# Performance work log

Hardware: AMD Instinct MI355X
Metric: run time of the kernel (lower is better)

## Reference

```python
import jax, jax.numpy as jnp
import numpy as np

B, FIN, FOUT, FH = 32, 32, 32, 64
H = W = 128
LAT = 512
K_IN, K_MID, K_OUT, K_SHORT = FH * FIN, FH * FH, FOUT * FH, FOUT * FIN
K_TOTAL = K_IN + K_MID + K_OUT + K_SHORT + FH + FH + FOUT + FOUT  # 9408


def setup_inputs() -> dict:
    key = jax.random.key(0)
    ks = jax.random.split(key, 20)
    def rn(k, shape, scale=None):
        s = scale if scale is not None else 1.0 / np.sqrt(shape[-1])
        return jax.random.normal(k, shape, dtype=jnp.float32) * s
    return {
        "x": jax.random.normal(ks[0], (B, FIN, H, W), dtype=jnp.float32),
        "lat": jax.random.normal(ks[1], (B, LAT), dtype=jnp.float32),
        "w0": rn(ks[2], (LAT, LAT)), "b0": rn(ks[3], (LAT,), 0.02),
        "w1a": rn(ks[4], (2 * LAT, LAT)), "b1a": rn(ks[5], (2 * LAT,), 0.02),
        "w1b": rn(ks[6], (LAT, 2 * LAT)), "b1b": rn(ks[7], (LAT,), 0.02),
        "w1s": rn(ks[8], (LAT, LAT)), "b1s": rn(ks[9], (LAT,), 0.02),
        "w2a": rn(ks[10], (2 * LAT, LAT)), "b2a": rn(ks[11], (2 * LAT,), 0.02),
        "w2b": rn(ks[12], (K_TOTAL, 2 * LAT)), "b2b": rn(ks[13], (K_TOTAL,), 0.02),
        "w2s": rn(ks[14], (K_TOTAL, LAT)), "b2s": rn(ks[15], (K_TOTAL,), 0.02),
        "wfa": rn(ks[16], (K_TOTAL, K_TOTAL)), "bfa": rn(ks[17], (K_TOTAL,), 0.02),
    }


def _lrb(h, wa, ba, wb, bb, ws, bs):
    # LinearResidualBlock: shortcut + 2-layer MLP with ReLU
    return h @ ws.T + bs + jax.nn.relu(h @ wa.T + ba) @ wb.T + bb


def reference(x, lat, w0, b0, w1a, b1a, w1b, b1b, w1s, b1s,
              w2a, b2a, w2b, b2b, w2s, b2s, wfa, bfa):
    # hypernetwork: dyna_k then LinearFA (forward is a plain linear)
    h = lat @ w0.T + b0                              # [B, 512]
    h = _lrb(h, w1a, b1a, w1b, b1b, w1s, b1s)        # [B, 512]
    h = _lrb(h, w2a, b2a, w2b, b2b, w2s, b2s)        # [B, K_TOTAL]
    ks = h @ wfa.T + bfa                             # [B, K_TOTAL]

    sizes = [K_IN, K_MID, K_OUT, K_SHORT, FH, FH, FOUT, FOUT]
    offs = np.cumsum([0] + sizes)
    k_in = ks[:, offs[0]:offs[1]].reshape(B, FH, FIN)
    k_mid = ks[:, offs[1]:offs[2]].reshape(B, FH, FH)
    k_out = ks[:, offs[2]:offs[3]].reshape(B, FOUT, FH)
    k_short = ks[:, offs[3]:offs[4]].reshape(B, FOUT, FIN)
    b_in = ks[:, offs[4]:offs[5]][:, :, None, None]    # [B, FH, 1, 1]
    b_mid = ks[:, offs[5]:offs[6]][:, :, None, None]
    b_out = ks[:, offs[6]:offs[7]][:, :, None, None]   # [B, FOUT, 1, 1]
    b_short = ks[:, offs[7]:offs[8]][:, :, None, None]

    # per-sample 1x1 grouped convs == batched matmuls over channels
    xs = jnp.einsum('bihw,boi->bohw', x, k_short) + b_short
    xn = jax.nn.relu(jnp.einsum('bihw,boi->bohw', x, k_in) + b_in)
    xn = jax.nn.relu(jnp.einsum('bihw,boi->bohw', xn, k_mid) + b_mid)
    xn = jnp.einsum('bihw,boi->bohw', xn, k_out) + b_out
    return xn + xs
```

## Files before the change

### kernel.cpp

```cpp
#include <hip/hip_runtime.h>
#include <cstdint>

#define KT 9408
#define NT 256
#define KC 16

__global__ __launch_bounds__(256, 1) void gemm32_partial(
    const float* __restrict__ X1, const float* __restrict__ W1, int K1,
    const float* __restrict__ X2, const float* __restrict__ W2, int K2,
    float* __restrict__ partial, int O, int ksplit)
{
    __shared__ float Xs[KC][32];
    __shared__ float Wt[KC][NT];

    const int t      = threadIdx.x;
    const int o0     = blockIdx.x * NT;
    const int s      = blockIdx.y;
    const int kchunk = (K1 + K2) / ksplit;
    const int kbeg   = s * kchunk;
    const int kend   = kbeg + kchunk;
    const int lane   = t & 63;
    const int wv     = t >> 6;

    const int sr  = t >> 2;
    const int sc4 = (t & 3) << 2;

    float4 wpre[4];
    float  xpre[2];

    {
        int kc0 = kbeg;
#pragma unroll
        for (int p = 0; p < 4; ++p) {
            int r = sr + 64 * p;
            int o = o0 + r;
            int kg = kc0 + sc4;
            float4 v = make_float4(0.f, 0.f, 0.f, 0.f);
            if (o < O)
                v = (kg < K1) ? *(const float4*)&W1[(size_t)o * K1 + kg]
                              : *(const float4*)&W2[(size_t)o * K2 + (kg - K1)];
            wpre[p] = v;
        }
#pragma unroll
        for (int it = 0; it < 2; ++it) {
            int idx = t + 256 * it;
            int kg  = kc0 + (idx >> 5);
            int bb  = idx & 31;
            xpre[it] = (kg < K1) ? X1[(size_t)bb * K1 + kg]
                                 : X2[(size_t)bb * K2 + (kg - K1)];
        }
    }

    float acc[8][4];
#pragma unroll
    for (int bi = 0; bi < 8; bi++)
#pragma unroll
        for (int j = 0; j < 4; j++) acc[bi][j] = 0.f;

    for (int kc0 = kbeg; kc0 < kend; kc0 += KC) {
#pragma unroll
        for (int it = 0; it < 2; ++it) {
            int idx = t + 256 * it;
            Xs[idx >> 5][idx & 31] = xpre[it];
        }
#pragma unroll
        for (int p = 0; p < 4; ++p) {
            int r = sr + 64 * p;
            Wt[sc4 + 0][r] = wpre[p].x;
            Wt[sc4 + 1][r] = wpre[p].y;
            Wt[sc4 + 2][r] = wpre[p].z;
            Wt[sc4 + 3][r] = wpre[p].w;
        }
        __syncthreads();

        if (kc0 + KC < kend) {
            int kn = kc0 + KC;
#pragma unroll
            for (int p = 0; p < 4; ++p) {
                int r = sr + 64 * p;
                int o = o0 + r;
                int kg = kn + sc4;
                float4 v = make_float4(0.f, 0.f, 0.f, 0.f);
                if (o < O)
                    v = (kg < K1) ? *(const float4*)&W1[(size_t)o * K1 + kg]
                                  : *(const float4*)&W2[(size_t)o * K2 + (kg - K1)];
                wpre[p] = v;
            }
#pragma unroll
            for (int it = 0; it < 2; ++it) {
                int idx = t + 256 * it;
                int kg  = kn + (idx >> 5);
                int bb  = idx & 31;
                xpre[it] = (kg < K1) ? X1[(size_t)bb * K1 + kg]
                                     : X2[(size_t)bb * K2 + (kg - K1)];
            }
        }

#pragma unroll
        for (int c = 0; c < KC; c++) {
            float4 xa = *(const float4*)&Xs[c][wv * 8];
            float4 xb = *(const float4*)&Xs[c][wv * 8 + 4];
            float xv[8] = {xa.x, xa.y, xa.z, xa.w, xb.x, xb.y, xb.z, xb.w};
            float w[4];
#pragma unroll
            for (int j = 0; j < 4; j++) w[j] = Wt[c][lane + 64 * j];
#pragma unroll
            for (int bi = 0; bi < 8; bi++)
#pragma unroll
                for (int j = 0; j < 4; j++) acc[bi][j] += xv[bi] * w[j];
        }
        __syncthreads();
    }

#pragma unroll
    for (int bi = 0; bi < 8; bi++) {
        int b = wv * 8 + bi;
#pragma unroll
        for (int j = 0; j < 4; j++) {
            int o = o0 + lane + 64 * j;
            if (o < O)
                partial[((size_t)s * 32 + b) * O + o] = acc[bi][j];
        }
    }
}

__global__ __launch_bounds__(256) void reduce_bias(
    const float* __restrict__ partial, const float* __restrict__ bias1,
    const float* __restrict__ bias2, float* __restrict__ Y, int O, int relu,
    int ksplit)
{
    int idx = blockIdx.x * 256 + threadIdx.x;
    if (idx >= 32 * O) return;
    int b = idx / O, o = idx - b * O;
    float s = bias1[o] + (bias2 ? bias2[o] : 0.f);
    for (int k = 0; k < ksplit; k++)
        s += partial[((size_t)k * 32 + b) * O + o];
    Y[idx] = relu ? fmaxf(s, 0.f) : s;
}

typedef __attribute__((ext_vector_type(8))) short bf16x8;
typedef __attribute__((ext_vector_type(4))) float f32x4;

__device__ inline uint32_t pkbf(float lo, float hi) {
    uint32_t a = __builtin_bit_cast(uint32_t, lo);
    uint32_t b = __builtin_bit_cast(uint32_t, hi);
    a = (a + 0x7FFFu + ((a >> 16) & 1u)) >> 16;
    b = (b + 0x7FFFu + ((b >> 16) & 1u)) & 0xFFFF0000u;
    return a | b;
}

#define MFMA16(a, b, c) __builtin_amdgcn_mfma_f32_16x16x32_bf16(a, b, c, 0, 0, 0)

#define TPW 16

__global__ __launch_bounds__(256, 3) void conv_mfma(
    const float* __restrict__ x, const float* __restrict__ ks,
    float* __restrict__ out)
{
    const int t  = threadIdx.x;
    const int b  = blockIdx.y;
    const int l  = t & 63;
    const int g  = l >> 4;
    const int n  = l & 15;
    const int wid = blockIdx.x * 4 + (t >> 6);

    const float* __restrict__ kb = ks + (size_t)b * KT;
    const float* __restrict__ xbase = x + (size_t)b * 524288 + (size_t)(4 * g) * 16384 + n;
    float* __restrict__ obase = out + (size_t)b * 524288 + (size_t)(4 * g) * 16384 + n;

    float e[8];
    auto loadx = [&](int px0) {
        const float* p = xbase + px0;
        e[0] = p[0]; e[1] = p[16384]; e[2] = p[2 * 16384]; e[3] = p[3 * 16384];
        const float* q = p + (size_t)16 * 16384;
        e[4] = q[0]; e[5] = q[16384]; e[6] = q[2 * 16384]; e[7] = q[3 * 16384];
    };
    loadx(wid * TPW * 16);

    auto loadA = [&](const float* W, int ldw, int row0, int k0) -> bf16x8 {
        const float* p = W + (size_t)(row0 + n) * ldw + k0 + 4 * g;
        float4 lo = *(const float4*)p;
        float4 hi = *(const float4*)(p + 16);
        union { bf16x8 v; uint32_t u[4]; } r;
        r.u[0] = pkbf(lo.x, lo.y);
        r.u[1] = pkbf(lo.z, lo.w);
        r.u[2] = pkbf(hi.x, hi.y);
        r.u[3] = pkbf(hi.z, hi.w);
        return r.v;
    };
    auto loadBias = [&](int off) -> f32x4 {
        float4 v = *(const float4*)&kb[off + 4 * g];
        f32x4 r; r[0] = v.x; r[1] = v.y; r[2] = v.z; r[3] = v.w;
        return r;
    };

    bf16x8 ain[4], amid[4][2], aout[2][2], ashort[2];
#pragma unroll
    for (int rt = 0; rt < 4; ++rt) ain[rt] = loadA(kb, 32, 16 * rt, 0);
#pragma unroll
    for (int ot = 0; ot < 4; ++ot)
#pragma unroll
        for (int kf = 0; kf < 2; ++kf) amid[ot][kf] = loadA(kb + 2048, 64, 16 * ot, 32 * kf);
#pragma unroll
    for (int ot = 0; ot < 2; ++ot)
#pragma unroll
        for (int kf = 0; kf < 2; ++kf) aout[ot][kf] = loadA(kb + 6144, 64, 16 * ot, 32 * kf);
#pragma unroll
    for (int ot = 0; ot < 2; ++ot) ashort[ot] = loadA(kb + 8192, 32, 16 * ot, 0);

    f32x4 bin[4], bmid[4], bos[2];
#pragma unroll
    for (int rt = 0; rt < 4; ++rt) bin[rt] = loadBias(9216 + 16 * rt);
#pragma unroll
    for (int ot = 0; ot < 4; ++ot) bmid[ot] = loadBias(9280 + 16 * ot);
#pragma unroll
    for (int ot = 0; ot < 2; ++ot) {
        f32x4 a = loadBias(9344 + 16 * ot);
        f32x4 c = loadBias(9376 + 16 * ot);
#pragma unroll
        for (int r = 0; r < 4; ++r) a[r] += c[r];
        bos[ot] = a;
    }

#pragma unroll 1
    for (int it = 0; it < TPW; ++it) {
        const int px0 = (wid * TPW + it) * 16;

        union { bf16x8 v; uint32_t u[4]; } bx;
        bx.u[0] = pkbf(e[0], e[1]); bx.u[1] = pkbf(e[2], e[3]);
        bx.u[2] = pkbf(e[4], e[5]); bx.u[3] = pkbf(e[6], e[7]);

        if (it + 1 < TPW) loadx(px0 + 16);

        f32x4 h[4];
#pragma unroll
        for (int rt = 0; rt < 4; ++rt) {
            f32x4 acc = MFMA16(ain[rt], bx.v, bin[rt]);
#pragma unroll
            for (int r = 0; r < 4; ++r) acc[r] = fmaxf(acc[r], 0.f);
            h[rt] = acc;
        }
        union { bf16x8 v; uint32_t u[4]; } hb0, hb1;
        hb0.u[0] = pkbf(h[0][0], h[0][1]); hb0.u[1] = pkbf(h[0][2], h[0][3]);
        hb0.u[2] = pkbf(h[1][0], h[1][1]); hb0.u[3] = pkbf(h[1][2], h[1][3]);
        hb1.u[0] = pkbf(h[2][0], h[2][1]); hb1.u[1] = pkbf(h[2][2], h[2][3]);
        hb1.u[2] = pkbf(h[3][0], h[3][1]); hb1.u[3] = pkbf(h[3][2], h[3][3]);

        f32x4 m[4];
#pragma unroll
        for (int ot = 0; ot < 4; ++ot) {
            f32x4 acc = MFMA16(amid[ot][0], hb0.v, bmid[ot]);
            acc = MFMA16(amid[ot][1], hb1.v, acc);
#pragma unroll
            for (int r = 0; r < 4; ++r) acc[r] = fmaxf(acc[r], 0.f);
            m[ot] = acc;
        }
        union { bf16x8 v; uint32_t u[4]; } mb0, mb1;
        mb0.u[0] = pkbf(m[0][0], m[0][1]); mb0.u[1] = pkbf(m[0][2], m[0][3]);
        mb0.u[2] = pkbf(m[1][0], m[1][1]); mb0.u[3] = pkbf(m[1][2], m[1][3]);
        mb1.u[0] = pkbf(m[2][0], m[2][1]); mb1.u[1] = pkbf(m[2][2], m[2][3]);
        mb1.u[2] = pkbf(m[3][0], m[3][1]); mb1.u[3] = pkbf(m[3][2], m[3][3]);

#pragma unroll
        for (int ot = 0; ot < 2; ++ot) {
            f32x4 acc = MFMA16(ashort[ot], bx.v, bos[ot]);
            acc = MFMA16(aout[ot][0], mb0.v, acc);
            acc = MFMA16(aout[ot][1], mb1.v, acc);
            float* po = obase + (size_t)(16 * ot) * 16384 + px0;
            po[0]         = acc[0];
            po[16384]     = acc[1];
            po[2 * 16384] = acc[2];
            po[3 * 16384] = acc[3];
        }
    }
}

extern "C" void kernel_launch(void* const* d_in, const int* in_sizes, int n_in,
                              void* d_out, int out_size, void* d_ws, size_t ws_size,
                              hipStream_t stream)
{
    const float* x   = (const float*)d_in[0];
    const float* lat = (const float*)d_in[1];
    const float* w0  = (const float*)d_in[2];
    const float* b0  = (const float*)d_in[3];
    const float* w1a = (const float*)d_in[4];
    const float* b1a = (const float*)d_in[5];
    const float* w1b = (const float*)d_in[6];
    const float* b1b = (const float*)d_in[7];
    const float* w1s = (const float*)d_in[8];
    const float* b1s = (const float*)d_in[9];
    const float* w2a = (const float*)d_in[10];
    const float* b2a = (const float*)d_in[11];
    const float* w2b = (const float*)d_in[12];
    const float* b2b = (const float*)d_in[13];
    const float* w2s = (const float*)d_in[14];
    const float* b2s = (const float*)d_in[15];
    const float* wfa = (const float*)d_in[16];
    const float* bfa = (const float*)d_in[17];

    float* ws  = (float*)d_ws;
    float* h0  = ws;
    float* t1  = ws + 16384;
    float* h1  = ws + 49152;
    float* t2  = ws + 65536;
    float* h2  = ws + 98304;
    float* ksb = ws + 399360;
    float* pbuf = (float*)d_out;

    dim3 blk(256);
    auto g  = [](int O, int ks) { return dim3((unsigned)((O + NT - 1) / NT), (unsigned)ks); };
    auto rg = [](int O) { return dim3((unsigned)((32 * O + 255) / 256)); };

    gemm32_partial<<<g(512, 32), blk, 0, stream>>>(lat, w0, 512, nullptr, nullptr, 0, pbuf, 512, 32);
    reduce_bias<<<rg(512), blk, 0, stream>>>(pbuf, b0, nullptr, h0, 512, 0, 32);
    gemm32_partial<<<g(1024, 32), blk, 0, stream>>>(h0, w1a, 512, nullptr, nullptr, 0, pbuf, 1024, 32);
    reduce_bias<<<rg(1024), blk, 0, stream>>>(pbuf, b1a, nullptr, t1, 1024, 1, 32);
    gemm32_partial<<<g(512, 32), blk, 0, stream>>>(h0, w1s, 512, t1, w1b, 1024, pbuf, 512, 32);
    reduce_bias<<<rg(512), blk, 0, stream>>>(pbuf, b1s, b1b, h1, 512, 0, 32);
    gemm32_partial<<<g(1024, 32), blk, 0, stream>>>(h1, w2a, 512, nullptr, nullptr, 0, pbuf, 1024, 32);
    reduce_bias<<<rg(1024), blk, 0, stream>>>(pbuf, b2a, nullptr, t2, 1024, 1, 32);
    gemm32_partial<<<g(KT, 32), blk, 0, stream>>>(h1, w2s, 512, t2, w2b, 1024, pbuf, KT, 32);
    reduce_bias<<<rg(KT), blk, 0, stream>>>(pbuf, b2s, b2b, h2, KT, 0, 32);
    gemm32_partial<<<g(KT, 28), blk, 0, stream>>>(h2, wfa, KT, nullptr, nullptr, 0, pbuf, KT, 28);
    reduce_bias<<<rg(KT), blk, 0, stream>>>(pbuf, bfa, nullptr, ksb, KT, 0, 28);

    conv_mfma<<<dim3(16, 32), blk, 0, stream>>>(x, ksb, (float*)d_out);
}
```

Measured before the change: 299.1 us.

## Use split-bf16 MFMA for the two large hypernetwork GEMMs

Adds an MFMA GEMM kernel for the 32-row linear layers. Each weight chunk is converted to bf16, and each activation is split into a high and a low bf16 part so accuracy stays close to fp32. The two largest layers (the 1536->9408 residual output and the 9408x9408 LinearFA) use this kernel with much smaller k-splits, which shrinks the partial buffers and the reduce work. The weights are rounded to bf16, which loses some precision, and the wfa weight stream is still read straight from global memory without going through LDS.

```diff
diff --git a/kernel.cpp b/kernel.cpp
--- a/kernel.cpp
+++ b/kernel.cpp
@@ -148,8 +148,79 @@
     b = (b + 0x7FFFu + ((b >> 16) & 1u)) & 0xFFFF0000u;
     return a | b;
 }
+__device__ inline uint32_t pk_hi(float a, float b, float& ra, float& rb) {
+    uint32_t ua = __builtin_bit_cast(uint32_t, a);
+    uint32_t ub = __builtin_bit_cast(uint32_t, b);
+    uint32_t ha = (ua + 0x7FFFu + ((ua >> 16) & 1u)) & 0xFFFF0000u;
+    uint32_t hb = (ub + 0x7FFFu + ((ub >> 16) & 1u)) & 0xFFFF0000u;
+    ra = a - __builtin_bit_cast(float, ha);
+    rb = b - __builtin_bit_cast(float, hb);
+    return (ha >> 16) | hb;
+}
 
 #define MFMA16(a, b, c) __builtin_amdgcn_mfma_f32_16x16x32_bf16(a, b, c, 0, 0, 0)
+
+__global__ __launch_bounds__(256) void gemm32_mfma(
+    const float* __restrict__ X1, const float* __restrict__ W1, int K1,
+    const float* __restrict__ X2, const float* __restrict__ W2, int K2,
+    float* __restrict__ partial, int O, int ksplit)
+{
+    const int t  = threadIdx.x;
+    const int l  = t & 63;
+    const int g  = l >> 4;
+    const int n  = l & 15;
+    const int o0 = blockIdx.x * 64 + (t >> 6) * 16;
+    const int s  = blockIdx.y;
+    const int kchunk = (K1 + K2) / ksplit;
+    const int kbeg   = s * kchunk;
+    const int kend   = kbeg + kchunk;
+
+    f32x4 accA, accB;
+#pragma unroll
+    for (int r = 0; r < 4; ++r) { accA[r] = 0.f; accB[r] = 0.f; }
+
+#pragma unroll 2
+    for (int kc = kbeg; kc < kend; kc += 32) {
+        const float* Wr;  const float* Xb;  int kk; int ld;
+        if (kc < K1) { Wr = W1; Xb = X1; kk = kc;      ld = K1; }
+        else         { Wr = W2; Xb = X2; kk = kc - K1; ld = K2; }
+
+        const float* wp = Wr + (size_t)(o0 + n) * ld + kk + 4 * g;
+        float4 wlo = *(const float4*)wp;
+        float4 whi = *(const float4*)(wp + 16);
+        union { bf16x8 v; uint32_t u[4]; } wf;
+        wf.u[0] = pkbf(wlo.x, wlo.y); wf.u[1] = pkbf(wlo.z, wlo.w);
+        wf.u[2] = pkbf(whi.x, whi.y); wf.u[3] = pkbf(whi.z, whi.w);
+
+#pragma unroll
+        for (int bh = 0; bh < 2; ++bh) {
+            const float* xp = Xb + (size_t)(16 * bh + n) * ld + kk + 4 * g;
+            float4 xa = *(const float4*)xp;
+            float4 xb = *(const float4*)(xp + 16);
+            float r0, r1, r2, r3, r4, r5, r6, r7;
+            union { bf16x8 v; uint32_t u[4]; } xh, xl;
+            xh.u[0] = pk_hi(xa.x, xa.y, r0, r1);
+            xh.u[1] = pk_hi(xa.z, xa.w, r2, r3);
+            xh.u[2] = pk_hi(xb.x, xb.y, r4, r5);
+            xh.u[3] = pk_hi(xb.z, xb.w, r6, r7);
+            xl.u[0] = pkbf(r0, r1); xl.u[1] = pkbf(r2, r3);
+            xl.u[2] = pkbf(r4, r5); xl.u[3] = pkbf(r6, r7);
+            if (bh == 0) {
+                accA = MFMA16(xh.v, wf.v, accA);
+                accA = MFMA16(xl.v, wf.v, accA);
+            } else {
+                accB = MFMA16(xh.v, wf.v, accB);
+                accB = MFMA16(xl.v, wf.v, accB);
+            }
+        }
+    }
+
+#pragma unroll
+    for (int r = 0; r < 4; ++r) {
+        partial[((size_t)s * 32 + (4 * g + r)) * O + o0 + n]      = accA[r];
+        partial[((size_t)s * 32 + (16 + 4 * g + r)) * O + o0 + n] = accB[r];
+    }
+}
 
 #define TPW 16
 
@@ -308,21 +379,21 @@
     float* pbuf = (float*)d_out;
 
     dim3 blk(256);
-    auto g  = [](int O, int ks) { return dim3((unsigned)((O + NT - 1) / NT), (unsigned)ks); };
     auto rg = [](int O) { return dim3((unsigned)((32 * O + 255) / 256)); };
 
-    gemm32_partial<<<g(512, 32), blk, 0, stream>>>(lat, w0, 512, nullptr, nullptr, 0, pbuf, 512, 32);
+    gemm32_partial<<<dim3(2, 32), blk, 0, stream>>>(lat, w0, 512, nullptr, nullptr, 0, pbuf, 512, 32);
     reduce_bias<<<rg(512), blk, 0, stream>>>(pbuf, b0, nullptr, h0, 512, 0, 32);
-    gemm32_partial<<<g(1024, 32), blk, 0, stream>>>(h0, w1a, 512, nullptr, nullptr, 0, pbuf, 1024, 32);
+    gemm32_partial<<<dim3(4, 32), blk, 0, stream>>>(h0, w1a, 512, nullptr, nullptr, 0, pbuf, 1024, 32);
     reduce_bias<<<rg(1024), blk, 0, stream>>>(pbuf, b1a, nullptr, t1, 1024, 1, 32);
-    gemm32_partial<<<g(512, 32), blk, 0, stream>>>(h0, w1s, 512, t1, w1b, 1024, pbuf, 512, 32);
+    gemm32_partial<<<dim3(2, 32), blk, 0, stream>>>(h0, w1s, 512, t1, w1b, 1024, pbuf, 512, 32);
     reduce_bias<<<rg(512), blk, 0, stream>>>(pbuf, b1s, b1b, h1, 512, 0, 32);
-    gemm32_partial<<<g(1024, 32), blk, 0, stream>>>(h1, w2a, 512, nullptr, nullptr, 0, pbuf, 1024, 32);
+    gemm32_partial<<<dim3(4, 32), blk, 0, stream>>>(h1, w2a, 512, nullptr, nullptr, 0, pbuf, 1024, 32);
     reduce_bias<<<rg(1024), blk, 0, stream>>>(pbuf, b2a, nullptr, t2, 1024, 1, 32);
-    gemm32_partial<<<g(KT, 32), blk, 0, stream>>>(h1, w2s, 512, t2, w2b, 1024, pbuf, KT, 32);
-    reduce_bias<<<rg(KT), blk, 0, stream>>>(pbuf, b2s, b2b, h2, KT, 0, 32);
-    gemm32_partial<<<g(KT, 28), blk, 0, stream>>>(h2, wfa, KT, nullptr, nullptr, 0, pbuf, KT, 28);
-    reduce_bias<<<rg(KT), blk, 0, stream>>>(pbuf, bfa, nullptr, ksb, KT, 0, 28);
+
+    gemm32_mfma<<<dim3(147, 6), blk, 0, stream>>>(h1, w2s, 512, t2, w2b, 1024, pbuf, KT, 6);
+    reduce_bias<<<rg(KT), blk, 0, stream>>>(pbuf, b2s, b2b, h2, KT, 0, 6);
+    gemm32_mfma<<<dim3(147, 7), blk, 0, stream>>>(h2, wfa, KT, nullptr, nullptr, 0, pbuf, KT, 7);
+    reduce_bias<<<rg(KT), blk, 0, stream>>>(pbuf, bfa, nullptr, ksb, KT, 0, 7);
 
     conv_mfma<<<dim3(16, 32), blk, 0, stream>>>(x, ksb, (float*)d_out);
 }
```

After: 294.3 us. About the same (-1.6%).
